# Kernel optimization log

Measured on AMD Instinct MI355X. Metric: run time of the kernel, lower is better.

Reference implementation:

```python
import jax, jax.numpy as jnp
import numpy as np

GROUPSIZE = 4      # g: multivariate group size (d = groupsize - 2)
NB_GROUPS = 48     # f: number of expert groups / filters
CHANNELS = 128     # c: signal channels fed to the L operator
SCALE = 0.999
SLOPE = 1.0        # model_params['scaling']
LAMB_INIT = 0.1
EPS_OMEGA_INIT = -2.0


def proj_l1(x):
    """Euclidean projection onto the unit l1 ball along axis 1. x: [B,G,F,H,W]."""
    ax = jnp.abs(x)
    s = -jnp.sort(-ax, axis=1)                      # descending |x|
    cssv = jnp.cumsum(s, axis=1) - 1.0
    G = x.shape[1]
    k = jnp.arange(1, G + 1, dtype=x.dtype).reshape(1, G, 1, 1, 1)
    cond = s * k > cssv
    rho = jnp.sum(cond, axis=1, keepdims=True)       # number of active coords
    theta = jnp.take_along_axis(cssv, rho - 1, axis=1) / rho.astype(x.dtype)
    theta = jnp.maximum(theta, 0.0)
    proj = jnp.sign(x) * jnp.maximum(ax - theta, 0.0)
    inside = jnp.sum(ax, axis=1, keepdims=True) <= 1.0
    return jnp.where(inside, x, proj)


def _forward(x_noisy, sigma, Q_param, taus_param, lamb, eps_omega,
             mu_w1, mu_b1, mu_w2, mu_b2, mu_w3, mu_b3, Wf, n_iter):
    lamb_e = jnp.exp(lamb)
    eps_e = jnp.exp(eps_omega)

    # --- Q normalization + spectral norms (cached once per forward) ---
    Q = Q_param / jnp.maximum(jnp.sum(jnp.abs(Q_param), axis=2, keepdims=True), 1.0)
    Q_norms = jnp.linalg.svd(Q, compute_uv=False)[:, 0].reshape(-1, 1, 1)  # [F,1,1]
    Q_eff = Q / Q_norms ** 2
    taus = jnp.exp(jax.nn.relu(taus_param))          # [1,1,F,1,1]

    # --- per-batch noise-adaptive scaling via small MLP ---
    h = jax.nn.relu((sigma * 20.0 - 2.0) @ mu_w1 + mu_b1)
    h = jax.nn.relu(h @ mu_w2 + mu_b2)
    h = h @ mu_w3 + mu_b3                            # [B,F]
    scaling = jax.nn.relu(h * 0.05 + sigma) * SLOPE + 1e-9
    scaling = scaling.reshape(-1, 1, scaling.shape[-1], 1, 1)  # [B,1,F,1,1]

    def moreau(x):
        g = proj_l1(x)
        cost = jnp.max(jnp.abs(x - g), axis=1) + 0.5 * jnp.sum(g * g, axis=1)
        cost = cost[:, None]                         # [B,1,F,H,W]
        g = g + eps_e * x
        cost = cost + eps_e * 0.5 * jnp.sqrt(jnp.sum(x * x, axis=1, keepdims=True))
        return g, cost

    def activation(x):
        gc, cc = moreau(x)
        # orient: scale * einsum('flg,bgfhw->blfhw', Q/Q_norms^2, x), then /taus
        y = SCALE * jnp.einsum('flg,bgfhw->blfhw', Q_eff, x) / taus
        gcc, ccc = moreau(y)
        # unorient: scale * einsum with Q^T  (Q^T[f,l,g] = Q[f,g,l])
        gcc = SCALE * jnp.einsum('fgl,bgfhw->blfhw', Q, gcc)
        ccc = Q_norms ** 2 * (taus * ccc)
        return lamb_e * (gc - gcc), lamb_e * (cc - ccc)

    def reconstruct(x):
        Lx = jnp.einsum('gfc,bchw->bgfhw', Wf, x) / scaling
        g, cost = activation(Lx)
        g = jnp.einsum('gfc,bgfhw->bchw', Wf, g * scaling)   # adjoint L^T
        cost = jnp.sum(cost * scaling ** 2, axis=(1, 2, 3, 4))
        g = (x - x_noisy + g) / (1.0 + lamb_e * (1.0 + eps_e))
        cost = cost + 0.5 * jnp.sum((x - x_noisy) ** 2, axis=(1, 2, 3))
        return g, cost

    def step(x, _):
        g, _c = reconstruct(x)
        return x - g, None

    x_final, _ = jax.lax.scan(jax.checkpoint(step), x_noisy, jnp.arange(n_iter))
    return x_final


def setup_inputs() -> dict:
    key = jax.random.key(0)
    ks = jax.random.split(key, 8)
    B, C, H, W = 2, CHANNELS, 128, 128
    F_, G = NB_GROUPS, GROUPSIZE
    x_noisy = jax.random.normal(ks[0], (B, C, H, W), jnp.float32)
    sigma = jax.random.uniform(ks[1], (B, 1), jnp.float32)
    Q_param = jax.random.uniform(ks[2], (F_, G, G), jnp.float32) - 0.5
    taus_param = (LAMB_INIT / 2.0) * jnp.ones((1, 1, F_, 1, 1), jnp.float32)
    lamb = jnp.float32(LAMB_INIT)
    eps_omega = jnp.float32(EPS_OMEGA_INIT)
    mu_w1 = jax.random.normal(ks[3], (1, F_), jnp.float32)
    mu_b1 = jnp.zeros((F_,), jnp.float32)
    mu_w2 = jax.random.normal(ks[4], (F_, F_), jnp.float32) / np.float32(np.sqrt(F_))
    mu_b2 = jnp.zeros((F_,), jnp.float32)
    mu_w3 = jax.random.normal(ks[5], (F_, F_), jnp.float32) / np.float32(np.sqrt(F_))
    mu_b3 = jnp.zeros((F_,), jnp.float32)
    Wf = jax.random.normal(ks[6], (G, F_, C), jnp.float32) / np.float32(np.sqrt(C))
    return dict(x_noisy=x_noisy, sigma=sigma, Q_param=Q_param, taus_param=taus_param,
                lamb=lamb, eps_omega=eps_omega, mu_w1=mu_w1, mu_b1=mu_b1,
                mu_w2=mu_w2, mu_b2=mu_b2, mu_w3=mu_w3, mu_b3=mu_b3, Wf=Wf, n_iter=10)


def reference(x_noisy, sigma, Q_param, taus_param, lamb, eps_omega,
              mu_w1, mu_b1, mu_w2, mu_b2, mu_w3, mu_b3, Wf, n_iter):
    return _forward(x_noisy, sigma, Q_param, taus_param, lamb, eps_omega,
                    mu_w1, mu_b1, mu_w2, mu_b2, mu_w3, mu_b3, Wf, n_iter)
```

## Files before the change

kernel.cpp:

```cpp
#include <hip/hip_runtime.h>
#include <math.h>

#define F_ 48
#define C_ 128
#define HW 16384
#define SCALE_C 0.999f
#define TPB 256

typedef __attribute__((ext_vector_type(8))) short short8;
typedef __attribute__((ext_vector_type(4))) float floatx4;

#define P1_U 0
#define P2_U 98304
#define QEQN_F 98304
#define MISC_F (QEQN_F + 1536)
#define SINV_F (MISC_F + 2)
#define SLAM_F (SINV_F + 96)

#define XS 152
#define AS 104
#define QS 36

__device__ __forceinline__ unsigned short f2bf(float f) {
    unsigned u = __float_as_uint(f);
    unsigned r = u + 0x7fffu + ((u >> 16) & 1u);
    return (unsigned short)(r >> 16);
}
__device__ __forceinline__ float bf2f(unsigned short h) {
    return __uint_as_float(((unsigned)h) << 16);
}

__global__ void setup_math(const float* __restrict__ sigma,
                           const float* __restrict__ Qp,
                           const float* __restrict__ taus_p,
                           const float* __restrict__ lamb,
                           const float* __restrict__ eps_om,
                           const float* __restrict__ mw1, const float* __restrict__ mb1,
                           const float* __restrict__ mw2, const float* __restrict__ mb2,
                           const float* __restrict__ mw3, const float* __restrict__ mb3,
                           float* __restrict__ wsf)
{
    const int tid = threadIdx.x;
    if (tid < F_) {
        const int f = tid;
        float Qm[4][4];
        for (int g = 0; g < 4; ++g) {
            float s = 0.f;
            for (int l = 0; l < 4; ++l) s += fabsf(Qp[f * 16 + g * 4 + l]);
            float d = fmaxf(s, 1.0f);
            for (int l = 0; l < 4; ++l) Qm[g][l] = Qp[f * 16 + g * 4 + l] / d;
        }
        double A[4][4];
        for (int i = 0; i < 4; ++i)
            for (int j = 0; j < 4; ++j) {
                double s = 0.0;
                for (int g = 0; g < 4; ++g) s += (double)Qm[g][i] * (double)Qm[g][j];
                A[i][j] = s;
            }
        double M[4][4];
        for (int i = 0; i < 4; ++i) for (int j = 0; j < 4; ++j) M[i][j] = A[i][j];
        for (int it = 0; it < 30; ++it) {
            double T[4][4]; double mx = 0.0;
            for (int i = 0; i < 4; ++i)
                for (int j = 0; j < 4; ++j) {
                    double s = 0.0;
                    for (int k = 0; k < 4; ++k) s += M[i][k] * M[k][j];
                    T[i][j] = s;
                    double a = fabs(s); if (a > mx) mx = a;
                }
            if (mx < 1e-300) break;
            double inv = 1.0 / mx;
            for (int i = 0; i < 4; ++i) for (int j = 0; j < 4; ++j) M[i][j] = T[i][j] * inv;
        }
        int jb = 0; double bn = -1.0;
        for (int j = 0; j < 4; ++j) {
            double nn = 0.0;
            for (int i = 0; i < 4; ++i) nn += M[i][j] * M[i][j];
            if (nn > bn) { bn = nn; jb = j; }
        }
        double v[4]; for (int i = 0; i < 4; ++i) v[i] = M[i][jb];
        double Av[4];
        for (int i = 0; i < 4; ++i) {
            double s = 0.0;
            for (int j = 0; j < 4; ++j) s += A[i][j] * v[j];
            Av[i] = s;
        }
        double vv = 0.0, vav = 0.0;
        for (int i = 0; i < 4; ++i) { vv += v[i] * v[i]; vav += v[i] * Av[i]; }
        float lamf = (float)((vv > 0.0) ? (vav / vv) : 0.0);
        float tau = expf(fmaxf(taus_p[f], 0.0f));
        float qsv = SCALE_C / tau;
        for (int l = 0; l < 4; ++l)
            for (int g = 0; g < 4; ++g)
                wsf[QEQN_F + f * 32 + l * 4 + g] = qsv * Qm[l][g] / lamf;
        for (int g = 0; g < 4; ++g)
            for (int l = 0; l < 4; ++l)
                wsf[QEQN_F + f * 32 + 16 + g * 4 + l] = SCALE_C * Qm[g][l];
    }
    if (tid >= 48 && tid < 50) {
        const int b = tid - 48;
        float lamb_e = expf(lamb[0]);
        float sg = sigma[b];
        float t = sg * 20.0f - 2.0f;
        float h1[F_], h2[F_];
        for (int j = 0; j < F_; ++j) h1[j] = fmaxf(t * mw1[j] + mb1[j], 0.0f);
        for (int j = 0; j < F_; ++j) {
            float s = mb2[j];
            for (int k = 0; k < F_; ++k) s += h1[k] * mw2[k * F_ + j];
            h2[j] = fmaxf(s, 0.0f);
        }
        for (int j = 0; j < F_; ++j) {
            float s = mb3[j];
            for (int k = 0; k < F_; ++k) s += h2[k] * mw3[k * F_ + j];
            float sc = fmaxf(s * 0.05f + sg, 0.0f) + 1e-9f;
            wsf[SINV_F + b * F_ + j] = 1.0f / sc;
            wsf[SLAM_F + b * F_ + j] = lamb_e * sc;
        }
    }
    if (tid == 50) {
        float lamb_e = expf(lamb[0]);
        float eps_e = expf(eps_om[0]);
        wsf[MISC_F + 0] = eps_e;
        wsf[MISC_F + 1] = 1.0f / (1.0f + lamb_e * (1.0f + eps_e));
    }
}

__global__ void setup_pack(const float* __restrict__ Wf, float* __restrict__ wsf)
{
    unsigned short* wsu = (unsigned short*)wsf;
    const int gtid = blockIdx.x * TPB + threadIdx.x;
    for (int i = gtid; i < 49152; i += gridDim.x * TPB) {
        if (i < 24576) {
            int j = i & 7, lane = (i >> 3) & 63;
            int t = i >> 9;
            int ks = t & 3, mt = t >> 2;
            int m = lane & 15, q = lane >> 4;
            int r = mt * 16 + m;
            int c = ks * 32 + q * 8 + j;
            int f = r >> 2, g = r & 3;
            float w = Wf[(g * F_ + f) * C_ + c];
#pragma unroll
            for (int b = 0; b < 2; ++b) {
                float v = w * wsf[SINV_F + b * F_ + f];
                unsigned short h = (unsigned short)(__float_as_uint(v) >> 16);
                float lo = v - bf2f(h);
                unsigned short l = (unsigned short)(__float_as_uint(lo) >> 16);
                wsu[P1_U + ((((b * 2 + 0) * 12 + mt) * 4 + ks) * 64 + lane) * 8 + j] = h;
                wsu[P1_U + ((((b * 2 + 1) * 12 + mt) * 4 + ks) * 64 + lane) * 8 + j] = l;
            }
        } else {
            int ii = i - 24576;
            int j = ii & 7, lane = (ii >> 3) & 63;
            int t = ii >> 9;
            int ks = t % 6, cmt = t / 6;
            int m = lane & 15, q = lane >> 4;
            int cch = cmt * 16 + m;
            int r = ks * 32 + q * 8 + j;
            int f = r >> 2, g = r & 3;
            float w = Wf[(g * F_ + f) * C_ + cch];
#pragma unroll
            for (int b = 0; b < 2; ++b) {
                float v = w * wsf[SLAM_F + b * F_ + f];
                unsigned short h = (unsigned short)(__float_as_uint(v) >> 16);
                float lo = v - bf2f(h);
                unsigned short l = (unsigned short)(__float_as_uint(lo) >> 16);
                wsu[P2_U + ((((b * 2 + 0) * 8 + cmt) * 6 + ks) * 64 + lane) * 8 + j] = h;
                wsu[P2_U + ((((b * 2 + 1) * 8 + cmt) * 6 + ks) * 64 + lane) * 8 + j] = l;
            }
        }
    }
}

__device__ __forceinline__ void proj4(const float v[4], float o[4]) {
    float a0 = fabsf(v[0]), a1 = fabsf(v[1]), a2 = fabsf(v[2]), a3 = fabsf(v[3]);
    float sum = a0 + a1 + a2 + a3;
    float t0 = fmaxf(a0, a1), u0 = fminf(a0, a1);
    float t1 = fmaxf(a2, a3), u1 = fminf(a2, a3);
    float s0 = fmaxf(t0, t1), m0 = fminf(t0, t1);
    float m1 = fmaxf(u0, u1), s3 = fminf(u0, u1);
    float s1 = fmaxf(m1, m0), s2 = fminf(m1, m0);
    float c2 = s0 + s1, c3 = c2 + s2, c4 = c3 + s3;
    float th = s0 - 1.0f, rh = 1.0f;
    if (s1 * 2.0f > c2 - 1.0f) { th = c2 - 1.0f; rh = 2.0f; }
    if (s2 * 3.0f > c3 - 1.0f) { th = c3 - 1.0f; rh = 3.0f; }
    if (s3 * 4.0f > c4 - 1.0f) { th = c4 - 1.0f; rh = 4.0f; }
    float theta = fmaxf(th / rh, 0.0f);
    bool inside = (sum <= 1.0f);
#pragma unroll
    for (int g = 0; g < 4; ++g) {
        float ag = fabsf(v[g]);
        float pg = copysignf(fmaxf(ag - theta, 0.0f), v[g]);
        o[g] = inside ? v[g] : pg;
    }
}

__global__ __launch_bounds__(TPB, 4) void mfoe_main(
    const float* __restrict__ xnoisy,
    const float* __restrict__ wsf,
    float* __restrict__ out,
    const int* __restrict__ n_iter_p)
{
    __shared__ __align__(16) unsigned short sXH[32 * XS];
    __shared__ __align__(16) unsigned short sXL[32 * XS];
    __shared__ __align__(16) unsigned short sACT[32 * AS];
    __shared__ __align__(16) float sQ[F_ * QS];

    const int tid = threadIdx.x;
    const int lane = tid & 63;
    const int wv = __builtin_amdgcn_readfirstlane(tid >> 6);
    const int n = lane & 15;
    const int q = lane >> 4;
    const int blk = blockIdx.x;
    const int b = blk >> 9;
    const int pix0 = (blk & 511) << 5;

    const float* __restrict__ xin = xnoisy + b * (C_ * HW) + pix0;
    float* __restrict__ oimg = out + b * (C_ * HW) + pix0;
    const unsigned short* __restrict__ wsu = (const unsigned short*)wsf;
    const int niter = *n_iter_p;

    if (niter == 0) {
        for (int i = tid; i < C_ * 32; i += TPB) {
            int p = i & 31, c = i >> 5;
            oimg[c * HW + p] = xin[c * HW + p];
        }
        return;
    }

    for (int i = tid; i < C_ * 32; i += TPB) {
        int p = i & 31, c = i >> 5;
        float v = xin[c * HW + p];
        unsigned short h = (unsigned short)(__float_as_uint(v) >> 16);
        float lo = v - bf2f(h);
        sXH[p * XS + c] = h;
        sXL[p * XS + c] = (unsigned short)(__float_as_uint(lo) >> 16);
    }
    for (int i = tid; i < F_ * 32; i += TPB)
        sQ[(i >> 5) * QS + (i & 31)] = wsf[QEQN_F + i];

    float xnr[16];
#pragma unroll
    for (int j = 0; j < 4; ++j) {
        int jw = wv * 4 + j, cmt = jw >> 1, nt = jw & 1;
        int p = nt * 16 + n;
#pragma unroll
        for (int reg = 0; reg < 4; ++reg)
            xnr[j * 4 + reg] = xin[(cmt * 16 + q * 4 + reg) * HW + p];
    }
    const float eps_e = wsf[MISC_F + 0];
    const float invden = wsf[MISC_F + 1];

    for (int it = 0; it < niter; ++it) {
        floatx4 acc2[4];
#pragma unroll
        for (int j = 0; j < 4; ++j) acc2[j] = (floatx4){0.f, 0.f, 0.f, 0.f};

#pragma unroll 1
        for (int h = 0; h < 2; ++h) {
            __syncthreads();
#pragma unroll 1
            for (int j = 0; j < 3; ++j) {
                int jw = wv * 3 + j, mtl = jw >> 1, nt = jw & 1;
                int mt = h * 6 + mtl;
                int p = nt * 16 + n;
                floatx4 acc = (floatx4){0.f, 0.f, 0.f, 0.f};
                const short8* aHp = (const short8*)(wsu + P1_U + (((b * 2 + 0) * 12 + mt) * 4) * 512 + lane * 8);
                const short8* aLp = (const short8*)(wsu + P1_U + (((b * 2 + 1) * 12 + mt) * 4) * 512 + lane * 8);
#pragma unroll
                for (int ks = 0; ks < 4; ++ks) {
                    short8 aH = aHp[ks * 64];
                    short8 aL = aLp[ks * 64];
                    short8 bH = *(const short8*)&sXH[p * XS + ks * 32 + q * 8];
                    short8 bL = *(const short8*)&sXL[p * XS + ks * 32 + q * 8];
                    acc = __builtin_amdgcn_mfma_f32_16x16x32_bf16(aH, bH, acc, 0, 0, 0);
                    acc = __builtin_amdgcn_mfma_f32_16x16x32_bf16(aH, bL, acc, 0, 0, 0);
                    acc = __builtin_amdgcn_mfma_f32_16x16x32_bf16(aL, bH, acc, 0, 0, 0);
                }
                int f = h * 24 + mtl * 4 + q;
                float qv[32];
#pragma unroll
                for (int k = 0; k < 8; ++k)
                    *(floatx4*)&qv[4 * k] = *(const floatx4*)&sQ[f * QS + 4 * k];
                float v[4] = {acc[0], acc[1], acc[2], acc[3]};
                float pv[4]; proj4(v, pv);
                float y[4];
#pragma unroll
                for (int l = 0; l < 4; ++l)
                    y[l] = fmaf(qv[l * 4 + 0], v[0], fmaf(qv[l * 4 + 1], v[1],
                           fmaf(qv[l * 4 + 2], v[2], qv[l * 4 + 3] * v[3])));
                float py[4]; proj4(y, py);
                float m2[4];
#pragma unroll
                for (int g = 0; g < 4; ++g) m2[g] = fmaf(eps_e, y[g], py[g]);
                unsigned pk0, pk1;
                {
                    float a0, a1;
                    float gcc0 = fmaf(qv[16 + 0], m2[0], fmaf(qv[16 + 4], m2[1],
                                 fmaf(qv[16 + 8], m2[2], qv[16 + 12] * m2[3])));
                    a0 = fmaf(eps_e, v[0], pv[0]) - gcc0;
                    float gcc1 = fmaf(qv[17 + 0], m2[0], fmaf(qv[17 + 4], m2[1],
                                 fmaf(qv[17 + 8], m2[2], qv[17 + 12] * m2[3])));
                    a1 = fmaf(eps_e, v[1], pv[1]) - gcc1;
                    pk0 = ((unsigned)f2bf(a1) << 16) | f2bf(a0);
                    float gcc2 = fmaf(qv[18 + 0], m2[0], fmaf(qv[18 + 4], m2[1],
                                 fmaf(qv[18 + 8], m2[2], qv[18 + 12] * m2[3])));
                    a0 = fmaf(eps_e, v[2], pv[2]) - gcc2;
                    float gcc3 = fmaf(qv[19 + 0], m2[0], fmaf(qv[19 + 4], m2[1],
                                 fmaf(qv[19 + 8], m2[2], qv[19 + 12] * m2[3])));
                    a1 = fmaf(eps_e, v[3], pv[3]) - gcc3;
                    pk1 = ((unsigned)f2bf(a1) << 16) | f2bf(a0);
                }
                unsigned long long pk = ((unsigned long long)pk1 << 32) | pk0;
                *(unsigned long long*)&sACT[p * AS + mtl * 16 + q * 4] = pk;
            }
            __syncthreads();
#pragma unroll
            for (int j = 0; j < 4; ++j) {
                int jw = wv * 4 + j, cmt = jw >> 1, nt = jw & 1;
                int p = nt * 16 + n;
                const short8* a2H = (const short8*)(wsu + P2_U + (((b * 2 + 0) * 8 + cmt) * 6 + h * 3) * 512 + lane * 8);
                const short8* a2L = (const short8*)(wsu + P2_U + (((b * 2 + 1) * 8 + cmt) * 6 + h * 3) * 512 + lane * 8);
                floatx4 a = acc2[j];
#pragma unroll
                for (int ksl = 0; ksl < 3; ++ksl) {
                    short8 aH = a2H[ksl * 64];
                    short8 aL = a2L[ksl * 64];
                    short8 bA = *(const short8*)&sACT[p * AS + ksl * 32 + q * 8];
                    a = __builtin_amdgcn_mfma_f32_16x16x32_bf16(aH, bA, a, 0, 0, 0);
                    a = __builtin_amdgcn_mfma_f32_16x16x32_bf16(aL, bA, a, 0, 0, 0);
                }
                acc2[j] = a;
            }
        }
        const bool last = (it == niter - 1);
#pragma unroll
        for (int j = 0; j < 4; ++j) {
            int jw = wv * 4 + j, cmt = jw >> 1, nt = jw & 1;
            int p = nt * 16 + n;
            int cb = cmt * 16 + q * 4;
            unsigned long long oh = *(const unsigned long long*)&sXH[p * XS + cb];
            unsigned long long ol = *(const unsigned long long*)&sXL[p * XS + cb];
            unsigned long long nh = 0ull, nl = 0ull;
#pragma unroll
            for (int reg = 0; reg < 4; ++reg) {
                float xo = bf2f((unsigned short)(oh >> (16 * reg))) +
                           bf2f((unsigned short)(ol >> (16 * reg)));
                float nx = xo - (xo - xnr[j * 4 + reg] + acc2[j][reg]) * invden;
                if (last) oimg[(cb + reg) * HW + p] = nx;
                unsigned short hh = (unsigned short)(__float_as_uint(nx) >> 16);
                float lo = nx - bf2f(hh);
                unsigned short ll = (unsigned short)(__float_as_uint(lo) >> 16);
                nh |= ((unsigned long long)hh) << (16 * reg);
                nl |= ((unsigned long long)ll) << (16 * reg);
            }
            *(unsigned long long*)&sXH[p * XS + cb] = nh;
            *(unsigned long long*)&sXL[p * XS + cb] = nl;
        }
    }
}

extern "C" void kernel_launch(void* const* d_in, const int* in_sizes, int n_in,
                              void* d_out, int out_size, void* d_ws, size_t ws_size,
                              hipStream_t stream) {
    const float* x_noisy = (const float*)d_in[0];
    const float* sigma   = (const float*)d_in[1];
    const float* Qp      = (const float*)d_in[2];
    const float* taus_p  = (const float*)d_in[3];
    const float* lamb    = (const float*)d_in[4];
    const float* eps_om  = (const float*)d_in[5];
    const float* mw1     = (const float*)d_in[6];
    const float* mb1     = (const float*)d_in[7];
    const float* mw2     = (const float*)d_in[8];
    const float* mb2     = (const float*)d_in[9];
    const float* mw3     = (const float*)d_in[10];
    const float* mb3     = (const float*)d_in[11];
    const float* Wf      = (const float*)d_in[12];
    const int*   n_iter  = (const int*)d_in[13];
    float* out = (float*)d_out;
    float* ws  = (float*)d_ws;

    hipLaunchKernelGGL(setup_math, dim3(1), dim3(64), 0, stream,
                       sigma, Qp, taus_p, lamb, eps_om,
                       mw1, mb1, mw2, mb2, mw3, mb3, ws);
    hipLaunchKernelGGL(setup_pack, dim3(192), dim3(TPB), 0, stream, Wf, ws);
    hipLaunchKernelGGL(mfoe_main, dim3(1024), dim3(TPB), 0, stream,
                       x_noisy, ws, out, n_iter);
}
```

Measured before the change: 333.1 us.

## Merge setup kernels and restructure main loop with single-pass activation and packed math

Fuses the two setup kernels into one launch where every block recomputes the small MLP scaling into shared memory, avoiding a dependent kernel launch. The main kernel now computes all 12 filter tiles of activations before one second GEMM over the full K of 192, instead of two halves with extra barriers. The iterate is kept in fp32 registers rather than reconstructed from the hi/lo bf16 pair each iteration. It also uses packed two-wide float FMAs and perm-based bf16 splitting, hoists the Q loads per tile, and changes shared-memory strides. In exchange, shared activation storage is larger and the MLP is recomputed redundantly in each of the 64 setup blocks.

```diff
diff --git a/kernel.cpp b/kernel.cpp
--- a/kernel.cpp
+++ b/kernel.cpp
@@ -9,16 +9,15 @@
 
 typedef __attribute__((ext_vector_type(8))) short short8;
 typedef __attribute__((ext_vector_type(4))) float floatx4;
+typedef __attribute__((ext_vector_type(2))) float v2;
+typedef __attribute__((ext_vector_type(2))) unsigned int uint2v;
 
 #define P1_U 0
 #define P2_U 98304
 #define QEQN_F 98304
 #define MISC_F (QEQN_F + 1536)
-#define SINV_F (MISC_F + 2)
-#define SLAM_F (SINV_F + 96)
-
-#define XS 152
-#define AS 104
+#define XS 136
+#define AS 200
 #define QS 36
 
 __device__ __forceinline__ unsigned short f2bf(float f) {
@@ -30,73 +29,22 @@
     return __uint_as_float(((unsigned)h) << 16);
 }
 
-__global__ void setup_math(const float* __restrict__ sigma,
-                           const float* __restrict__ Qp,
-                           const float* __restrict__ taus_p,
-                           const float* __restrict__ lamb,
-                           const float* __restrict__ eps_om,
-                           const float* __restrict__ mw1, const float* __restrict__ mb1,
-                           const float* __restrict__ mw2, const float* __restrict__ mb2,
-                           const float* __restrict__ mw3, const float* __restrict__ mb3,
-                           float* __restrict__ wsf)
+__global__ void setup_all(const float* __restrict__ sigma,
+                          const float* __restrict__ Qp,
+                          const float* __restrict__ taus_p,
+                          const float* __restrict__ lamb,
+                          const float* __restrict__ eps_om,
+                          const float* __restrict__ mw1, const float* __restrict__ mb1,
+                          const float* __restrict__ mw2, const float* __restrict__ mb2,
+                          const float* __restrict__ mw3, const float* __restrict__ mb3,
+                          const float* __restrict__ Wf,
+                          float* __restrict__ wsf)
 {
+    __shared__ float sInv[2][F_];
+    __shared__ float sLam[2][F_];
     const int tid = threadIdx.x;
-    if (tid < F_) {
-        const int f = tid;
-        float Qm[4][4];
-        for (int g = 0; g < 4; ++g) {
-            float s = 0.f;
-            for (int l = 0; l < 4; ++l) s += fabsf(Qp[f * 16 + g * 4 + l]);
-            float d = fmaxf(s, 1.0f);
-            for (int l = 0; l < 4; ++l) Qm[g][l] = Qp[f * 16 + g * 4 + l] / d;
-        }
-        double A[4][4];
-        for (int i = 0; i < 4; ++i)
-            for (int j = 0; j < 4; ++j) {
-                double s = 0.0;
-                for (int g = 0; g < 4; ++g) s += (double)Qm[g][i] * (double)Qm[g][j];
-                A[i][j] = s;
-            }
-        double M[4][4];
-        for (int i = 0; i < 4; ++i) for (int j = 0; j < 4; ++j) M[i][j] = A[i][j];
-        for (int it = 0; it < 30; ++it) {
-            double T[4][4]; double mx = 0.0;
-            for (int i = 0; i < 4; ++i)
-                for (int j = 0; j < 4; ++j) {
-                    double s = 0.0;
-                    for (int k = 0; k < 4; ++k) s += M[i][k] * M[k][j];
-                    T[i][j] = s;
-                    double a = fabs(s); if (a > mx) mx = a;
-                }
-            if (mx < 1e-300) break;
-            double inv = 1.0 / mx;
-            for (int i = 0; i < 4; ++i) for (int j = 0; j < 4; ++j) M[i][j] = T[i][j] * inv;
-        }
-        int jb = 0; double bn = -1.0;
-        for (int j = 0; j < 4; ++j) {
-            double nn = 0.0;
-            for (int i = 0; i < 4; ++i) nn += M[i][j] * M[i][j];
-            if (nn > bn) { bn = nn; jb = j; }
-        }
-        double v[4]; for (int i = 0; i < 4; ++i) v[i] = M[i][jb];
-        double Av[4];
-        for (int i = 0; i < 4; ++i) {
-            double s = 0.0;
-            for (int j = 0; j < 4; ++j) s += A[i][j] * v[j];
-            Av[i] = s;
-        }
-        double vv = 0.0, vav = 0.0;
-        for (int i = 0; i < 4; ++i) { vv += v[i] * v[i]; vav += v[i] * Av[i]; }
-        float lamf = (float)((vv > 0.0) ? (vav / vv) : 0.0);
-        float tau = expf(fmaxf(taus_p[f], 0.0f));
-        float qsv = SCALE_C / tau;
-        for (int l = 0; l < 4; ++l)
-            for (int g = 0; g < 4; ++g)
-                wsf[QEQN_F + f * 32 + l * 4 + g] = qsv * Qm[l][g] / lamf;
-        for (int g = 0; g < 4; ++g)
-            for (int l = 0; l < 4; ++l)
-                wsf[QEQN_F + f * 32 + 16 + g * 4 + l] = SCALE_C * Qm[g][l];
-    }
+    unsigned short* wsu = (unsigned short*)wsf;
+
     if (tid >= 48 && tid < 50) {
         const int b = tid - 48;
         float lamb_e = expf(lamb[0]);
@@ -113,23 +61,77 @@
             float s = mb3[j];
             for (int k = 0; k < F_; ++k) s += h2[k] * mw3[k * F_ + j];
             float sc = fmaxf(s * 0.05f + sg, 0.0f) + 1e-9f;
-            wsf[SINV_F + b * F_ + j] = 1.0f / sc;
-            wsf[SLAM_F + b * F_ + j] = lamb_e * sc;
-        }
-    }
-    if (tid == 50) {
-        float lamb_e = expf(lamb[0]);
-        float eps_e = expf(eps_om[0]);
-        wsf[MISC_F + 0] = eps_e;
-        wsf[MISC_F + 1] = 1.0f / (1.0f + lamb_e * (1.0f + eps_e));
-    }
-}
-
-__global__ void setup_pack(const float* __restrict__ Wf, float* __restrict__ wsf)
-{
-    unsigned short* wsu = (unsigned short*)wsf;
-    const int gtid = blockIdx.x * TPB + threadIdx.x;
-    for (int i = gtid; i < 49152; i += gridDim.x * TPB) {
+            sInv[b][j] = 1.0f / sc;
+            sLam[b][j] = lamb_e * sc;
+        }
+    }
+    if (blockIdx.x == 0) {
+        if (tid < F_) {
+            const int f = tid;
+            float Qm[4][4];
+            for (int g = 0; g < 4; ++g) {
+                float s = 0.f;
+                for (int l = 0; l < 4; ++l) s += fabsf(Qp[f * 16 + g * 4 + l]);
+                float d = fmaxf(s, 1.0f);
+                for (int l = 0; l < 4; ++l) Qm[g][l] = Qp[f * 16 + g * 4 + l] / d;
+            }
+            double A[4][4];
+            for (int i = 0; i < 4; ++i)
+                for (int j = 0; j < 4; ++j) {
+                    double s = 0.0;
+                    for (int g = 0; g < 4; ++g) s += (double)Qm[g][i] * (double)Qm[g][j];
+                    A[i][j] = s;
+                }
+            double M[4][4];
+            for (int i = 0; i < 4; ++i) for (int j = 0; j < 4; ++j) M[i][j] = A[i][j];
+            for (int it = 0; it < 30; ++it) {
+                double T[4][4]; double mx = 0.0;
+                for (int i = 0; i < 4; ++i)
+                    for (int j = 0; j < 4; ++j) {
+                        double s = 0.0;
+                        for (int k = 0; k < 4; ++k) s += M[i][k] * M[k][j];
+                        T[i][j] = s;
+                        double a = fabs(s); if (a > mx) mx = a;
+                    }
+                if (mx < 1e-300) break;
+                double inv = 1.0 / mx;
+                for (int i = 0; i < 4; ++i) for (int j = 0; j < 4; ++j) M[i][j] = T[i][j] * inv;
+            }
+            int jb = 0; double bn = -1.0;
+            for (int j = 0; j < 4; ++j) {
+                double nn = 0.0;
+                for (int i = 0; i < 4; ++i) nn += M[i][j] * M[i][j];
+                if (nn > bn) { bn = nn; jb = j; }
+            }
+            double v[4]; for (int i = 0; i < 4; ++i) v[i] = M[i][jb];
+            double Av[4];
+            for (int i = 0; i < 4; ++i) {
+                double s = 0.0;
+                for (int j = 0; j < 4; ++j) s += A[i][j] * v[j];
+                Av[i] = s;
+            }
+            double vv = 0.0, vav = 0.0;
+            for (int i = 0; i < 4; ++i) { vv += v[i] * v[i]; vav += v[i] * Av[i]; }
+            float lamf = (float)((vv > 0.0) ? (vav / vv) : 0.0);
+            float tau = expf(fmaxf(taus_p[f], 0.0f));
+            float qsv = SCALE_C / tau;
+            for (int g = 0; g < 4; ++g) {
+                for (int l = 0; l < 4; ++l)
+                    wsf[QEQN_F + f * 32 + 4 * g + l] = qsv * Qm[l][g] / lamf;
+                for (int l = 0; l < 4; ++l)
+                    wsf[QEQN_F + f * 32 + 16 + 4 * g + l] = SCALE_C * Qm[g][l];
+            }
+        }
+        if (tid == 50) {
+            float lamb_e = expf(lamb[0]);
+            float eps_e = expf(eps_om[0]);
+            wsf[MISC_F + 0] = eps_e;
+            wsf[MISC_F + 1] = 1.0f / (1.0f + lamb_e * (1.0f + eps_e));
+        }
+    }
+    __syncthreads();
+
+    for (int i = blockIdx.x * TPB + tid; i < 49152; i += gridDim.x * TPB) {
         if (i < 24576) {
             int j = i & 7, lane = (i >> 3) & 63;
             int t = i >> 9;
@@ -141,7 +143,7 @@
             float w = Wf[(g * F_ + f) * C_ + c];
 #pragma unroll
             for (int b = 0; b < 2; ++b) {
-                float v = w * wsf[SINV_F + b * F_ + f];
+                float v = w * sInv[b][f];
                 unsigned short h = (unsigned short)(__float_as_uint(v) >> 16);
                 float lo = v - bf2f(h);
                 unsigned short l = (unsigned short)(__float_as_uint(lo) >> 16);
@@ -160,7 +162,7 @@
             float w = Wf[(g * F_ + f) * C_ + cch];
 #pragma unroll
             for (int b = 0; b < 2; ++b) {
-                float v = w * wsf[SLAM_F + b * F_ + f];
+                float v = w * sLam[b][f];
                 unsigned short h = (unsigned short)(__float_as_uint(v) >> 16);
                 float lo = v - bf2f(h);
                 unsigned short l = (unsigned short)(__float_as_uint(lo) >> 16);
@@ -194,6 +196,18 @@
     }
 }
 
+__device__ __forceinline__ v2 fma2(v2 a, v2 b, v2 c) {
+    return __builtin_elementwise_fma(a, b, c);
+}
+
+__device__ __forceinline__ void split2(v2 nx, unsigned& hp, unsigned& lp) {
+    hp = __builtin_amdgcn_perm(__float_as_uint(nx.y), __float_as_uint(nx.x), 0x07060302u);
+    v2 hif = {__uint_as_float(__float_as_uint(nx.x) & 0xffff0000u),
+              __uint_as_float(__float_as_uint(nx.y) & 0xffff0000u)};
+    v2 lo = nx - hif;
+    lp = __builtin_amdgcn_perm(__float_as_uint(lo.y), __float_as_uint(lo.x), 0x07060302u);
+}
+
 __global__ __launch_bounds__(TPB, 4) void mfoe_main(
     const float* __restrict__ xnoisy,
     const float* __restrict__ wsf,
@@ -227,45 +241,53 @@
         return;
     }
 
-    for (int i = tid; i < C_ * 32; i += TPB) {
-        int p = i & 31, c = i >> 5;
-        float v = xin[c * HW + p];
-        unsigned short h = (unsigned short)(__float_as_uint(v) >> 16);
-        float lo = v - bf2f(h);
-        sXH[p * XS + c] = h;
-        sXL[p * XS + c] = (unsigned short)(__float_as_uint(lo) >> 16);
-    }
-    for (int i = tid; i < F_ * 32; i += TPB)
-        sQ[(i >> 5) * QS + (i & 31)] = wsf[QEQN_F + i];
-
-    float xnr[16];
+    v2 xr2[8], xn2[8];
 #pragma unroll
     for (int j = 0; j < 4; ++j) {
         int jw = wv * 4 + j, cmt = jw >> 1, nt = jw & 1;
         int p = nt * 16 + n;
 #pragma unroll
-        for (int reg = 0; reg < 4; ++reg)
-            xnr[j * 4 + reg] = xin[(cmt * 16 + q * 4 + reg) * HW + p];
-    }
+        for (int r = 0; r < 2; ++r) {
+            int c = cmt * 16 + q * 4 + 2 * r;
+            v2 t = {xin[c * HW + p], xin[(c + 1) * HW + p]};
+            xn2[j * 2 + r] = t;
+            xr2[j * 2 + r] = t;
+        }
+    }
+    for (int i = tid; i < F_ * 32; i += TPB)
+        sQ[(i >> 5) * QS + (i & 31)] = wsf[QEQN_F + i];
+
+#pragma unroll
+    for (int j = 0; j < 4; ++j) {
+        int jw = wv * 4 + j, cmt = jw >> 1, nt = jw & 1;
+        int p = nt * 16 + n;
+        int cb = cmt * 16 + q * 4;
+        unsigned h01, l01, h23, l23;
+        split2(xr2[j * 2 + 0], h01, l01);
+        split2(xr2[j * 2 + 1], h23, l23);
+        *(uint2v*)&sXH[p * XS + cb] = (uint2v){h01, h23};
+        *(uint2v*)&sXL[p * XS + cb] = (uint2v){l01, l23};
+    }
+
     const float eps_e = wsf[MISC_F + 0];
     const float invden = wsf[MISC_F + 1];
 
     for (int it = 0; it < niter; ++it) {
-        floatx4 acc2[4];
-#pragma unroll
-        for (int j = 0; j < 4; ++j) acc2[j] = (floatx4){0.f, 0.f, 0.f, 0.f};
-
+        __syncthreads();
 #pragma unroll 1
-        for (int h = 0; h < 2; ++h) {
-            __syncthreads();
-#pragma unroll 1
-            for (int j = 0; j < 3; ++j) {
-                int jw = wv * 3 + j, mtl = jw >> 1, nt = jw & 1;
-                int mt = h * 6 + mtl;
-                int p = nt * 16 + n;
+        for (int jj = 0; jj < 3; ++jj) {
+            const int mt = wv * 3 + jj;
+            const int f = mt * 4 + q;
+            floatx4 qf[8];
+#pragma unroll
+            for (int k = 0; k < 8; ++k)
+                qf[k] = *(const floatx4*)&sQ[f * QS + 4 * k];
+            const short8* aHp = (const short8*)(wsu + P1_U + (((b * 2 + 0) * 12 + mt) * 4) * 512 + lane * 8);
+            const short8* aLp = (const short8*)(wsu + P1_U + (((b * 2 + 1) * 12 + mt) * 4) * 512 + lane * 8);
+#pragma unroll
+            for (int nt = 0; nt < 2; ++nt) {
+                const int p = nt * 16 + n;
                 floatx4 acc = (floatx4){0.f, 0.f, 0.f, 0.f};
-                const short8* aHp = (const short8*)(wsu + P1_U + (((b * 2 + 0) * 12 + mt) * 4) * 512 + lane * 8);
-                const short8* aLp = (const short8*)(wsu + P1_U + (((b * 2 + 1) * 12 + mt) * 4) * 512 + lane * 8);
 #pragma unroll
                 for (int ks = 0; ks < 4; ++ks) {
                     short8 aH = aHp[ks * 64];
@@ -276,85 +298,85 @@
                     acc = __builtin_amdgcn_mfma_f32_16x16x32_bf16(aH, bL, acc, 0, 0, 0);
                     acc = __builtin_amdgcn_mfma_f32_16x16x32_bf16(aL, bH, acc, 0, 0, 0);
                 }
-                int f = h * 24 + mtl * 4 + q;
-                float qv[32];
-#pragma unroll
-                for (int k = 0; k < 8; ++k)
-                    *(floatx4*)&qv[4 * k] = *(const floatx4*)&sQ[f * QS + 4 * k];
                 float v[4] = {acc[0], acc[1], acc[2], acc[3]};
                 float pv[4]; proj4(v, pv);
-                float y[4];
-#pragma unroll
-                for (int l = 0; l < 4; ++l)
-                    y[l] = fmaf(qv[l * 4 + 0], v[0], fmaf(qv[l * 4 + 1], v[1],
-                           fmaf(qv[l * 4 + 2], v[2], qv[l * 4 + 3] * v[3])));
+                v2 y01 = qf[0].xy * v[0];
+                v2 y23 = qf[0].zw * v[0];
+                y01 = fma2(qf[1].xy, (v2){v[1], v[1]}, y01);
+                y23 = fma2(qf[1].zw, (v2){v[1], v[1]}, y23);
+                y01 = fma2(qf[2].xy, (v2){v[2], v[2]}, y01);
+                y23 = fma2(qf[2].zw, (v2){v[2], v[2]}, y23);
+                y01 = fma2(qf[3].xy, (v2){v[3], v[3]}, y01);
+                y23 = fma2(qf[3].zw, (v2){v[3], v[3]}, y23);
+                float y[4] = {y01.x, y01.y, y23.x, y23.y};
                 float py[4]; proj4(y, py);
                 float m2[4];
 #pragma unroll
                 for (int g = 0; g < 4; ++g) m2[g] = fmaf(eps_e, y[g], py[g]);
-                unsigned pk0, pk1;
-                {
-                    float a0, a1;
-                    float gcc0 = fmaf(qv[16 + 0], m2[0], fmaf(qv[16 + 4], m2[1],
-                                 fmaf(qv[16 + 8], m2[2], qv[16 + 12] * m2[3])));
-                    a0 = fmaf(eps_e, v[0], pv[0]) - gcc0;
-                    float gcc1 = fmaf(qv[17 + 0], m2[0], fmaf(qv[17 + 4], m2[1],
-                                 fmaf(qv[17 + 8], m2[2], qv[17 + 12] * m2[3])));
-                    a1 = fmaf(eps_e, v[1], pv[1]) - gcc1;
-                    pk0 = ((unsigned)f2bf(a1) << 16) | f2bf(a0);
-                    float gcc2 = fmaf(qv[18 + 0], m2[0], fmaf(qv[18 + 4], m2[1],
-                                 fmaf(qv[18 + 8], m2[2], qv[18 + 12] * m2[3])));
-                    a0 = fmaf(eps_e, v[2], pv[2]) - gcc2;
-                    float gcc3 = fmaf(qv[19 + 0], m2[0], fmaf(qv[19 + 4], m2[1],
-                                 fmaf(qv[19 + 8], m2[2], qv[19 + 12] * m2[3])));
-                    a1 = fmaf(eps_e, v[3], pv[3]) - gcc3;
-                    pk1 = ((unsigned)f2bf(a1) << 16) | f2bf(a0);
-                }
-                unsigned long long pk = ((unsigned long long)pk1 << 32) | pk0;
-                *(unsigned long long*)&sACT[p * AS + mtl * 16 + q * 4] = pk;
-            }
-            __syncthreads();
-#pragma unroll
-            for (int j = 0; j < 4; ++j) {
-                int jw = wv * 4 + j, cmt = jw >> 1, nt = jw & 1;
-                int p = nt * 16 + n;
-                const short8* a2H = (const short8*)(wsu + P2_U + (((b * 2 + 0) * 8 + cmt) * 6 + h * 3) * 512 + lane * 8);
-                const short8* a2L = (const short8*)(wsu + P2_U + (((b * 2 + 1) * 8 + cmt) * 6 + h * 3) * 512 + lane * 8);
-                floatx4 a = acc2[j];
-#pragma unroll
-                for (int ksl = 0; ksl < 3; ++ksl) {
-                    short8 aH = a2H[ksl * 64];
-                    short8 aL = a2L[ksl * 64];
-                    short8 bA = *(const short8*)&sACT[p * AS + ksl * 32 + q * 8];
-                    a = __builtin_amdgcn_mfma_f32_16x16x32_bf16(aH, bA, a, 0, 0, 0);
-                    a = __builtin_amdgcn_mfma_f32_16x16x32_bf16(aL, bA, a, 0, 0, 0);
-                }
-                acc2[j] = a;
-            }
+                v2 g01 = qf[4].xy * m2[0];
+                v2 g23 = qf[4].zw * m2[0];
+                g01 = fma2(qf[5].xy, (v2){m2[1], m2[1]}, g01);
+                g23 = fma2(qf[5].zw, (v2){m2[1], m2[1]}, g23);
+                g01 = fma2(qf[6].xy, (v2){m2[2], m2[2]}, g01);
+                g23 = fma2(qf[6].zw, (v2){m2[2], m2[2]}, g23);
+                g01 = fma2(qf[7].xy, (v2){m2[3], m2[3]}, g01);
+                g23 = fma2(qf[7].zw, (v2){m2[3], m2[3]}, g23);
+                float a0 = fmaf(eps_e, v[0], pv[0]) - g01.x;
+                float a1 = fmaf(eps_e, v[1], pv[1]) - g01.y;
+                float a2 = fmaf(eps_e, v[2], pv[2]) - g23.x;
+                float a3 = fmaf(eps_e, v[3], pv[3]) - g23.y;
+                unsigned pk0 = ((unsigned)f2bf(a1) << 16) | f2bf(a0);
+                unsigned pk1 = ((unsigned)f2bf(a3) << 16) | f2bf(a2);
+                *(uint2v*)&sACT[p * AS + mt * 16 + q * 4] = (uint2v){pk0, pk1};
+            }
+        }
+        __syncthreads();
+        floatx4 acc2[4];
+#pragma unroll
+        for (int j = 0; j < 4; ++j) acc2[j] = (floatx4){0.f, 0.f, 0.f, 0.f};
+#pragma unroll
+        for (int j = 0; j < 4; ++j) {
+            int jw = wv * 4 + j, cmt = jw >> 1, nt = jw & 1;
+            int p = nt * 16 + n;
+            const short8* a2H = (const short8*)(wsu + P2_U + (((b * 2 + 0) * 8 + cmt) * 6) * 512 + lane * 8);
+            const short8* a2L = (const short8*)(wsu + P2_U + (((b * 2 + 1) * 8 + cmt) * 6) * 512 + lane * 8);
+            floatx4 a = acc2[j];
+#pragma unroll
+            for (int ks = 0; ks < 6; ++ks) {
+                short8 aH = a2H[ks * 64];
+                short8 aL = a2L[ks * 64];
+                short8 bA = *(const short8*)&sACT[p * AS + ks * 32 + q * 8];
+                a = __builtin_amdgcn_mfma_f32_16x16x32_bf16(aH, bA, a, 0, 0, 0);
+                a = __builtin_amdgcn_mfma_f32_16x16x32_bf16(aL, bA, a, 0, 0, 0);
+            }
+            acc2[j] = a;
         }
         const bool last = (it == niter - 1);
+        const v2 dv = {invden, invden};
 #pragma unroll
         for (int j = 0; j < 4; ++j) {
             int jw = wv * 4 + j, cmt = jw >> 1, nt = jw & 1;
             int p = nt * 16 + n;
             int cb = cmt * 16 + q * 4;
-            unsigned long long oh = *(const unsigned long long*)&sXH[p * XS + cb];
-            unsigned long long ol = *(const unsigned long long*)&sXL[p * XS + cb];
-            unsigned long long nh = 0ull, nl = 0ull;
-#pragma unroll
-            for (int reg = 0; reg < 4; ++reg) {
-                float xo = bf2f((unsigned short)(oh >> (16 * reg))) +
-                           bf2f((unsigned short)(ol >> (16 * reg)));
-                float nx = xo - (xo - xnr[j * 4 + reg] + acc2[j][reg]) * invden;
-                if (last) oimg[(cb + reg) * HW + p] = nx;
-                unsigned short hh = (unsigned short)(__float_as_uint(nx) >> 16);
-                float lo = nx - bf2f(hh);
-                unsigned short ll = (unsigned short)(__float_as_uint(lo) >> 16);
-                nh |= ((unsigned long long)hh) << (16 * reg);
-                nl |= ((unsigned long long)ll) << (16 * reg);
-            }
-            *(unsigned long long*)&sXH[p * XS + cb] = nh;
-            *(unsigned long long*)&sXL[p * XS + cb] = nl;
+            unsigned hp[2], lp[2];
+#pragma unroll
+            for (int r = 0; r < 2; ++r) {
+                v2 xr = xr2[j * 2 + r];
+                v2 go = {acc2[j][2 * r], acc2[j][2 * r + 1]};
+                v2 t = (xr - xn2[j * 2 + r]) + go;
+                v2 nx = xr - t * dv;
+                xr2[j * 2 + r] = nx;
+                if (last) {
+                    oimg[(cb + 2 * r) * HW + p] = nx.x;
+                    oimg[(cb + 2 * r + 1) * HW + p] = nx.y;
+                } else {
+                    split2(nx, hp[r], lp[r]);
+                }
+            }
+            if (!last) {
+                *(uint2v*)&sXH[p * XS + cb] = (uint2v){hp[0], hp[1]};
+                *(uint2v*)&sXL[p * XS + cb] = (uint2v){lp[0], lp[1]};
+            }
         }
     }
 }
@@ -379,10 +401,9 @@
     float* out = (float*)d_out;
     float* ws  = (float*)d_ws;
 
-    hipLaunchKernelGGL(setup_math, dim3(1), dim3(64), 0, stream,
+    hipLaunchKernelGGL(setup_all, dim3(64), dim3(TPB), 0, stream,
                        sigma, Qp, taus_p, lamb, eps_om,
-                       mw1, mb1, mw2, mb2, mw3, mb3, ws);
-    hipLaunchKernelGGL(setup_pack, dim3(192), dim3(TPB), 0, stream, Wf, ws);
+                       mw1, mb1, mw2, mb2, mw3, mb3, Wf, ws);
     hipLaunchKernelGGL(mfoe_main, dim3(1024), dim3(TPB), 0, stream,
                        x_noisy, ws, out, n_iter);
 }
```

Result: slower. 532.8 us (+59.9%).
